# Performance work log

Measured on AMD Instinct MI355X. Metric: run time of the kernel, lower is better.

Reference implementation:

```python
import jax, jax.numpy as jnp
import numpy as np

NEG = -9.0e9  # the -9000000000.0 sentinel used by the torch code


def _masked_bidir_scores(first, second, fmask, smask):
    """Vectorized form of the BxB python double loop in score_grounding.
    first: (B,N,D), second: (B,L,D), fmask: (B,N), smask: (B,L).
    Returns sent_scores (B,B) and mention_scores (B,N,L) (= diagonal att)."""
    mask = fmask[:, None, :, None] * smask[None, :, None, :]          # (B,B,N,L)
    avg = jnp.where(mask != 0, mask, NEG)
    am_first = jax.nn.softmax(avg, axis=2)                            # softmax over N (dim=0 per pair)
    am_second = jax.nn.softmax(avg, axis=3)                           # softmax over L (dim=1 per pair)
    dot = jnp.einsum('ind,jld->ijnl', first, second)                  # (B,B,N,L)
    attm = dot * mask
    att = jnp.where(attm * mask != 0, attm, NEG)
    aw_first = jax.nn.softmax(att, axis=3) * mask                     # softmax(att, dim=-1)*mask
    aw_second = jnp.transpose(
        jax.nn.softmax(jnp.swapaxes(att, 2, 3), axis=3) * jnp.swapaxes(mask, 2, 3), (0, 1, 3, 2)
    )                                                                 # softmax(att.T,-1)*mask.T, transposed back
    sent = (jnp.sum(aw_first * att * am_first, axis=(2, 3))
            + jnp.sum(aw_second * att * am_second, axis=(2, 3)))      # (B,B)
    B = first.shape[0]
    mention = att[jnp.arange(B), jnp.arange(B)]                       # diagonal pairs (B,N,L)
    return sent, mention


def _pairwise_mlp(first, second, W1, b1, W2, b2, W3, b3):
    # SimplePairWiseClassifier: MLP over cat(first, second, first*second); dropout=0 (eval-deterministic)
    x = jnp.concatenate([first, second, first * second], axis=-1)     # (..., 3D)
    h = jax.nn.relu(x @ W1 + b1)
    h = jax.nn.relu(h @ W2 + b2)
    return (h @ W3 + b3)[..., 0]


def setup_inputs() -> dict:
    key = jax.random.key(0)
    ks = jax.random.split(key, 12)
    B, Nt, Ns, L, D, H = 32, 64, 48, 36, 1024, 1024

    def mask(k, n):
        m = (jax.random.uniform(k, (B, n)) < 0.85).astype(jnp.float32)
        return m.at[:, :2].set(1.0)  # guarantee no all-zero rows

    return {
        'text_embeddings': jax.random.normal(ks[0], (B, Nt, D), jnp.float32),
        'span_embeddings': jax.random.normal(ks[1], (B, Ns, D), jnp.float32),
        'image_embeddings': jax.random.normal(ks[2], (B, L, D), jnp.float32),
        'text_mask': mask(ks[3], Nt),
        'span_mask': mask(ks[4], Ns),
        'image_mask': mask(ks[5], L),
        'W1': jax.random.normal(ks[6], (3 * D, H), jnp.float32) * 0.02,
        'b1': jnp.zeros((H,), jnp.float32),
        'W2': jax.random.normal(ks[7], (H, H), jnp.float32) * 0.02,
        'b2': jnp.zeros((H,), jnp.float32),
        'W3': jax.random.normal(ks[8], (H, 1), jnp.float32) * 0.02,
        'b3': jnp.zeros((1,), jnp.float32),
    }


def reference(text_embeddings, span_embeddings, image_embeddings,
              text_mask, span_mask, image_mask, W1, b1, W2, b2, W3, b3):
    B, Ns, D = span_embeddings.shape
    # calculate_loss
    S, _ = _masked_bidir_scores(text_embeddings, image_embeddings, text_mask, image_mask)
    # span_emb.view(B, N, -1, D).mean(dim=2) is identity for (B,Ns,D)
    _, grounding_scores = _masked_bidir_scores(span_embeddings, image_embeddings, span_mask, image_mask)
    # score_text over all span pairs (itertools.combinations order == triu_indices k=1)
    fi, si = np.triu_indices(Ns, k=1)
    text_scores = _pairwise_mlp(span_embeddings[:, fi], span_embeddings[:, si],
                                W1, b1, W2, b2, W3, b3)               # (B, Ns*(Ns-1)/2)
    # contrastive retrieval loss over the BxB sentence-image score matrix
    loss = -(jnp.trace(jax.nn.log_softmax(S, axis=1))
             + jnp.trace(jax.nn.log_softmax(S.T, axis=1))) / B
    return loss, grounding_scores, text_scores
```

## Files before the change

kernel.cpp:

```cpp
#include <hip/hip_runtime.h>
#include <math.h>
#include <stdint.h>

#define B_    32
#define NT    64
#define NS    48
#define LI    36
#define D_    1024
#define H_    1024
#define NPAIR 1128
#define ROWS  (B_*NPAIR)
#define NEGV  -9.0e9f

typedef _Float16 half8 __attribute__((ext_vector_type(8)));
typedef float floatx4 __attribute__((ext_vector_type(4)));
typedef __attribute__((address_space(3))) uint32_t lds_u32;
typedef __attribute__((address_space(1))) const uint32_t glb_u32;

#define GLOAD16(src, dst) __builtin_amdgcn_global_load_lds((glb_u32*)(src), (lds_u32*)(dst), 16, 0, 0)

#define MMQ(QR, QC)                                                            \
  {                                                                            \
    _Pragma("unroll") for (int i = 0; i < 4; ++i) {                            \
      _Pragma("unroll") for (int j = 0; j < 2; ++j) {                          \
        acc[QR * 4 + i][QC * 2 + j] = __builtin_amdgcn_mfma_f32_16x16x32_f16(  \
            aF[i][0], bF[j][0], acc[QR * 4 + i][QC * 2 + j], 0, 0, 0);         \
        acc[QR * 4 + i][QC * 2 + j] = __builtin_amdgcn_mfma_f32_16x16x32_f16(  \
            aF[i][1], bF[j][1], acc[QR * 4 + i][QC * 2 + j], 0, 0, 0);         \
      }                                                                        \
    }                                                                          \
  }

__global__ __launch_bounds__(512, 2) void gemm1_8ph(
    const _Float16* __restrict__ spanH, const _Float16* __restrict__ W1cT,
    const float* __restrict__ AB1, const float* __restrict__ b1,
    _Float16* __restrict__ h1out,
    const int* __restrict__ idxF, const int* __restrict__ idxS) {
  __shared__ __align__(16) _Float16 sP[32768];
  __shared__ int sIF[256], sIS[256];

  const int orig = blockIdx.x;
  const int xcd = orig & 7, pos = orig >> 3;
  const int wg = (xcd < 4 ? xcd * 71 : 284 + (xcd - 4) * 70) + pos;
  const int rowBase = (wg >> 2) * 256;
  const int colBase = (wg & 3) * 256;

  const int t = threadIdx.x;
  const int wave = t >> 6, lane = t & 63;
  const int wq_r = wave >> 2, wq_c = wave & 3;
  const int l15 = lane & 15, l16 = lane >> 4;

  if (t < 256) { sIF[t] = idxF[rowBase + t]; sIS[t] = idxS[rowBase + t]; }
  __syncthreads();

  const int srow = t >> 3;
  const int slot = t & 7;
  const int wsw = ((slot ^ (srow & 7)) << 3);

  const int oF0a = sIF[srow] << 10,        oF0b = sIF[64 + srow] << 10;
  const int oS0a = sIS[srow] << 10,        oS0b = sIS[64 + srow] << 10;
  const int oF1a = sIF[128 + srow] << 10,  oF1b = sIF[192 + srow] << 10;
  const int oS1a = sIS[128 + srow] << 10,  oS1b = sIS[192 + srow] << 10;
  const int lcol = slot << 3;

  const _Float16* gB0a = W1cT + (size_t)(colBase + srow) * D_ + wsw;
  const _Float16* gB0b = W1cT + (size_t)(colBase + 64 + srow) * D_ + wsw;
  const _Float16* gB1a = W1cT + (size_t)(colBase + 128 + srow) * D_ + wsw;
  const _Float16* gB1b = W1cT + (size_t)(colBase + 192 + srow) * D_ + wsw;

  half8 rF0a, rF0b, rS0a, rS0b, rF1a, rF1b, rS1a, rS1b;

  #define ISSUE_FS0(kt) {                                            \
    const int kc = (((kt) & 15) << 6) + lcol;                        \
    rF0a = *(const half8*)(spanH + oF0a + kc);                       \
    rF0b = *(const half8*)(spanH + oF0b + kc);                       \
    rS0a = *(const half8*)(spanH + oS0a + kc);                       \
    rS0b = *(const half8*)(spanH + oS0b + kc); }
  #define ISSUE_FS1(kt) {                                            \
    const int kc = (((kt) & 15) << 6) + lcol;                        \
    rF1a = *(const half8*)(spanH + oF1a + kc);                       \
    rF1b = *(const half8*)(spanH + oF1b + kc);                       \
    rS1a = *(const half8*)(spanH + oS1a + kc);                       \
    rS1b = *(const half8*)(spanH + oS1b + kc); }
  #define WRITE_A0() {                                               \
    *(half8*)(sP + srow * 64 + wsw)        = rF0a * rS0a;            \
    *(half8*)(sP + 4096 + srow * 64 + wsw) = rF0b * rS0b; }
  #define WRITE_A1() {                                               \
    *(half8*)(sP + 8192 + srow * 64 + wsw)  = rF1a * rS1a;           \
    *(half8*)(sP + 12288 + srow * 64 + wsw) = rF1b * rS1b; }
  #define STG_B0(kt) {                                               \
    const int kc = (((kt) & 15) << 6);                               \
    GLOAD16(gB0a + kc, sP + 16384 + t * 8);                          \
    GLOAD16(gB0b + kc, sP + 20480 + t * 8); }
  #define STG_B1(kt) {                                               \
    const int kc = (((kt) & 15) << 6);                               \
    GLOAD16(gB1a + kc, sP + 24576 + t * 8);                          \
    GLOAD16(gB1b + kc, sP + 28672 + t * 8); }

  const int rsw = l15 & 7;
  const int aRd = (wq_r * 64 + l15) * 64;
  const int bRd = (wq_c * 32 + l15) * 64;
  const int rd0 = ((l16) ^ rsw) << 3;
  const int rd1 = ((4 + l16) ^ rsw) << 3;
  half8 aF[4][2], bF[2][2];
  floatx4 acc[8][4] = {};
  #define LDA(h) {                                                   \
    const _Float16* p = sP + (h) * 8192 + aRd;                       \
    _Pragma("unroll") for (int i = 0; i < 4; ++i) {                  \
      aF[i][0] = *(const half8*)(p + i * 1024 + rd0);                \
      aF[i][1] = *(const half8*)(p + i * 1024 + rd1); } }
  #define LDB(h) {                                                   \
    const _Float16* p = sP + 16384 + (h) * 8192 + bRd;               \
    _Pragma("unroll") for (int j = 0; j < 2; ++j) {                  \
      bF[j][0] = *(const half8*)(p + j * 1024 + rd0);                \
      bF[j][1] = *(const half8*)(p + j * 1024 + rd1); } }

  ISSUE_FS0(0); ISSUE_FS1(0); STG_B0(0);
  asm volatile("s_waitcnt vmcnt(6)" ::: "memory");
  WRITE_A0();
  asm volatile("s_waitcnt lgkmcnt(0)" ::: "memory");
  __builtin_amdgcn_sched_barrier(0);
  __builtin_amdgcn_s_barrier();

#pragma unroll 1
  for (int kt = 0; kt < 16; ++kt) {
    STG_B1(kt);
    ISSUE_FS0(kt + 1);
    asm volatile("s_waitcnt vmcnt(6)" ::: "memory");
    WRITE_A1();
    LDA(0); LDB(0);
    asm volatile("s_waitcnt lgkmcnt(0)" ::: "memory");
    __builtin_amdgcn_sched_barrier(0);
    __builtin_amdgcn_s_barrier();
    __builtin_amdgcn_s_setprio(1);
    MMQ(0, 0);
    __builtin_amdgcn_s_setprio(0);
    __builtin_amdgcn_s_barrier();
    ISSUE_FS1(kt + 1);
    LDA(1);
    __builtin_amdgcn_sched_barrier(0);
    __builtin_amdgcn_s_barrier();
    __builtin_amdgcn_s_setprio(1);
    MMQ(1, 0);
    __builtin_amdgcn_s_setprio(0);
    __builtin_amdgcn_s_barrier();
    STG_B0(kt + 1);
    asm volatile("s_waitcnt vmcnt(10)" ::: "memory");
    LDA(0); LDB(1);
    __builtin_amdgcn_sched_barrier(0);
    __builtin_amdgcn_s_barrier();
    __builtin_amdgcn_s_setprio(1);
    MMQ(0, 1);
    __builtin_amdgcn_s_setprio(0);
    __builtin_amdgcn_s_barrier();
    asm volatile("s_waitcnt vmcnt(6)" ::: "memory");
    WRITE_A0();
    LDA(1);
    asm volatile("s_waitcnt lgkmcnt(0)" ::: "memory");
    __builtin_amdgcn_sched_barrier(0);
    __builtin_amdgcn_s_barrier();
    __builtin_amdgcn_s_setprio(1);
    MMQ(1, 1);
    __builtin_amdgcn_s_setprio(0);
    __builtin_amdgcn_s_barrier();
  }

  float bv[2][2];
#pragma unroll
  for (int qc = 0; qc < 2; ++qc)
#pragma unroll
    for (int j = 0; j < 2; ++j)
      bv[qc][j] = b1[colBase + qc * 128 + wq_c * 32 + j * 16 + l15];
#pragma unroll
  for (int qr = 0; qr < 2; ++qr)
#pragma unroll
    for (int i = 0; i < 4; ++i)
#pragma unroll
      for (int q = 0; q < 4; ++q) {
        int rL = qr * 128 + wq_r * 64 + i * 16 + l16 * 4 + q;
        const float* ap = AB1 + (size_t)sIF[rL] * 2048;
        const float* bp = AB1 + (size_t)sIS[rL] * 2048 + 1024;
        size_t ro = (size_t)(rowBase + rL) * 1024;
#pragma unroll
        for (int qc = 0; qc < 2; ++qc)
#pragma unroll
          for (int j = 0; j < 2; ++j) {
            int c = colBase + qc * 128 + wq_c * 32 + j * 16 + l15;
            float v = acc[qr * 4 + i][qc * 2 + j][q] + ap[c] + bp[c] + bv[qc][j];
            h1out[ro + c] = (_Float16)fmaxf(v, 0.f);
          }
      }
}

__global__ __launch_bounds__(512, 2) void gemm2_8ph(
    const _Float16* __restrict__ Am, const _Float16* __restrict__ Bt,
    float* __restrict__ scores, const float* __restrict__ bias,
    const float* __restrict__ W3) {
  __shared__ __align__(16) _Float16 sP[65536];
  __shared__ float sRed[256][4];

  const int orig = blockIdx.x;
  const int xcd = orig & 7, pos = orig >> 3;
  const int wg = (xcd < 4 ? xcd * 71 : 284 + (xcd - 4) * 70) + pos;
  const int rowBase = (wg >> 2) * 256;
  const int colBase = (wg & 3) * 256;

  const int t = threadIdx.x;
  const int wave = t >> 6, lane = t & 63;
  const int wq_r = wave >> 2, wq_c = wave & 3;
  const int l15 = lane & 15, l16 = lane >> 4;
  const int sxor = l15 & 7;

  const int srow0 = t >> 3, srow1 = (512 + t) >> 3;
  const int lcol0 = ((t & 7) ^ (srow0 & 7)) << 3;
  const int lcol1 = (((512 + t) & 7) ^ (srow1 & 7)) << 3;
  const _Float16* aS0 = Am + (size_t)(rowBase + srow0) * D_ + lcol0;
  const _Float16* aS1 = Am + (size_t)(rowBase + srow1) * D_ + lcol1;
  const _Float16* bS0 = Bt + (size_t)(colBase + srow0) * D_ + lcol0;
  const _Float16* bS1 = Bt + (size_t)(colBase + srow1) * D_ + lcol1;

  auto stgA = [&](int kt, int h) {
    const int db = kt & 1;
    const size_t so = (size_t)(kt & 15) * 64 + (size_t)h * 128 * D_;
    _Float16* d = sP + ((db << 1) + h) * 8192;
    GLOAD16(aS0 + so, d + t * 8);
    GLOAD16(aS1 + so, d + 4096 + t * 8);
  };
  auto stgB = [&](int kt, int h) {
    const int db = kt & 1;
    const size_t so = (size_t)(kt & 15) * 64 + (size_t)h * 128 * D_;
    _Float16* d = sP + 32768 + ((db << 1) + h) * 8192;
    GLOAD16(bS0 + so, d + t * 8);
    GLOAD16(bS1 + so, d + 4096 + t * 8);
  };

  const int aRdRow = (wq_r * 64 + l15) * 64;
  const int bRdRow = (wq_c * 32 + l15) * 64;
  const int rdSlot0 = ((l16) ^ sxor) << 3;
  const int rdSlot1 = ((4 + l16) ^ sxor) << 3;

  half8 aF[4][2], bF[2][2];
  floatx4 acc[8][4] = {};

  auto ldA = [&](int db, int qr) {
    const _Float16* p = sP + ((db << 1) + qr) * 8192 + aRdRow;
#pragma unroll
    for (int i = 0; i < 4; ++i) {
      aF[i][0] = *(const half8*)(p + i * 1024 + rdSlot0);
      aF[i][1] = *(const half8*)(p + i * 1024 + rdSlot1);
    }
  };
  auto ldB = [&](int db, int qc) {
    const _Float16* p = sP + 32768 + ((db << 1) + qc) * 8192 + bRdRow;
#pragma unroll
    for (int j = 0; j < 2; ++j) {
      bF[j][0] = *(const half8*)(p + j * 1024 + rdSlot0);
      bF[j][1] = *(const half8*)(p + j * 1024 + rdSlot1);
    }
  };

  stgB(0, 0); stgA(0, 1); stgA(0, 0); stgB(0, 1); stgB(1, 0); stgA(1, 1);
  asm volatile("s_waitcnt vmcnt(4)" ::: "memory");
  __builtin_amdgcn_s_barrier();

#pragma unroll 1
  for (int kt = 0; kt < 16; ++kt) {
    const int db = kt & 1;
    const int kn1 = kt + 1, kn2 = kt + 2;
    ldA(db, 0); ldB(db, 0);
    stgA(kn1, 0);
    __builtin_amdgcn_sched_barrier(0);
    __builtin_amdgcn_s_barrier();
    __builtin_amdgcn_s_setprio(1);
    MMQ(0, 0);
    __builtin_amdgcn_s_setprio(0);
    __builtin_amdgcn_s_barrier();
    ldA(db, 1);
    stgB(kn1, 1);
    __builtin_amdgcn_sched_barrier(0);
    __builtin_amdgcn_s_barrier();
    __builtin_amdgcn_s_setprio(1);
    MMQ(1, 0);
    __builtin_amdgcn_s_setprio(0);
    __builtin_amdgcn_s_barrier();
    ldB(db, 1);
    stgB(kn2, 0);
    __builtin_amdgcn_sched_barrier(0);
    __builtin_amdgcn_s_barrier();
    __builtin_amdgcn_s_setprio(1);
    MMQ(1, 1);
    __builtin_amdgcn_s_setprio(0);
    __builtin_amdgcn_s_barrier();
    ldA(db, 0);
    stgA(kn2, 1);
    __builtin_amdgcn_sched_barrier(0);
    asm volatile("s_waitcnt vmcnt(4)" ::: "memory");
    __builtin_amdgcn_s_barrier();
    __builtin_amdgcn_s_setprio(1);
    MMQ(0, 1);
    __builtin_amdgcn_s_setprio(0);
    __builtin_amdgcn_s_barrier();
  }

  float bv[2][2], wv[2][2];
#pragma unroll
  for (int qc = 0; qc < 2; ++qc)
#pragma unroll
    for (int j = 0; j < 2; ++j) {
      int c = colBase + qc * 128 + wq_c * 32 + j * 16 + l15;
      bv[qc][j] = bias[c];
      wv[qc][j] = W3[c];
    }
#pragma unroll
  for (int qr = 0; qr < 2; ++qr)
#pragma unroll
    for (int i = 0; i < 4; ++i)
#pragma unroll
      for (int q = 0; q < 4; ++q) {
        float s = 0.f;
#pragma unroll
        for (int qc = 0; qc < 2; ++qc)
#pragma unroll
          for (int j = 0; j < 2; ++j)
            s += fmaxf(acc[qr * 4 + i][qc * 2 + j][q] + bv[qc][j], 0.f) * wv[qc][j];
        s += __shfl_xor(s, 1); s += __shfl_xor(s, 2);
        s += __shfl_xor(s, 4); s += __shfl_xor(s, 8);
        if (l15 == 0)
          sRed[qr * 128 + wq_r * 64 + i * 16 + l16 * 4 + q][wq_c] = s;
      }
  __syncthreads();
  if (t < 256)
    atomicAdd(&scores[rowBase + t],
              sRed[t][0] + sRed[t][1] + sRed[t][2] + sRed[t][3]);
}

__device__ __forceinline__ void gemm_body(
    const _Float16* __restrict__ A, const _Float16* __restrict__ Bt,
    float* __restrict__ Cf, int N, int K, int rowBase, int colBase) {
  __shared__ __align__(16) _Float16 sA[8192];
  __shared__ __align__(16) _Float16 sB[8192];
  const int tid = threadIdx.x;
  const int lane = tid & 63;
  const int wave = tid >> 6;
  const int wr = wave >> 1, wc = wave & 1;
  const int l15 = lane & 15, l16 = lane >> 4;
  const int rsw = (l15 >> 1) & 3;
  const int sRow = tid >> 2;
  const int swz8 = (((tid & 3) ^ ((tid >> 3) & 3)) << 3);
  const _Float16* gA = A + (size_t)(rowBase + sRow) * K + swz8;
  const _Float16* gB = Bt + (size_t)(colBase + sRow) * K + swz8;
  _Float16* lA = sA + tid * 8;
  _Float16* lB = sB + tid * 8;

  floatx4 acc[4][4] = {};
  for (int k0 = 0; k0 < K; k0 += 64) {
    GLOAD16(gA + k0,               lA);
    GLOAD16(gA + 64 * K + k0,      lA + 2048);
    GLOAD16(gA + k0 + 32,          lA + 4096);
    GLOAD16(gA + 64 * K + k0 + 32, lA + 6144);
    GLOAD16(gB + k0,               lB);
    GLOAD16(gB + 64 * K + k0,      lB + 2048);
    GLOAD16(gB + k0 + 32,          lB + 4096);
    GLOAD16(gB + 64 * K + k0 + 32, lB + 6144);
    __syncthreads();
#pragma unroll
    for (int h = 0; h < 2; ++h) {
      const int hb = h * 4096;
      half8 aF[4], bF[4];
#pragma unroll
      for (int i = 0; i < 4; ++i)
        aF[i] = *(const half8*)&sA[hb + (wr * 64 + i * 16 + l15) * 32 + ((l16 ^ rsw) << 3)];
#pragma unroll
      for (int j = 0; j < 4; ++j)
        bF[j] = *(const half8*)&sB[hb + (wc * 64 + j * 16 + l15) * 32 + ((l16 ^ rsw) << 3)];
#pragma unroll
      for (int i = 0; i < 4; ++i)
#pragma unroll
        for (int j = 0; j < 4; ++j)
          acc[i][j] = __builtin_amdgcn_mfma_f32_16x16x32_f16(aF[i], bF[j], acc[i][j], 0, 0, 0);
    }
    __syncthreads();
  }
#pragma unroll
  for (int i = 0; i < 4; ++i)
#pragma unroll
    for (int q = 0; q < 4; ++q) {
      int r = rowBase + wr * 64 + i * 16 + l16 * 4 + q;
#pragma unroll
      for (int j = 0; j < 4; ++j) {
        int c = colBase + wc * 64 + j * 16 + l15;
        Cf[(size_t)r * N + c] = acc[i][j][q];
      }
    }
}

__global__ __launch_bounds__(256) void gemm_trio(
    const _Float16* __restrict__ textH, const _Float16* __restrict__ imgH,
    const _Float16* __restrict__ spanH, const _Float16* __restrict__ W1abT,
    float* __restrict__ dotTI, float* __restrict__ dotSI, float* __restrict__ AB1) {
  int bid = blockIdx.x;
  if (bid < 144)      gemm_body(textH, imgH, dotTI, 1152, D_, (bid / 9) * 128, (bid % 9) * 128);
  else if (bid < 252) { int b = bid - 144; gemm_body(spanH, imgH, dotSI, 1152, D_, (b / 9) * 128, (b % 9) * 128); }
  else                { int b = bid - 252; gemm_body(spanH, W1abT, AB1, 2048, D_, (b / 16) * 128, (b % 16) * 128); }
}

__global__ __launch_bounds__(256) void cvt_all(
    const float* __restrict__ text, const float* __restrict__ span,
    const float* __restrict__ img, _Float16* __restrict__ textH,
    _Float16* __restrict__ spanH, _Float16* __restrict__ imgH) {
  long long i = (long long)blockIdx.x * 256 + threadIdx.x;
  const float* src; _Float16* dst; long long off;
  if (i < 262144)      { src = text; dst = textH; off = i; }
  else if (i < 458752) { src = span; dst = spanH; off = i - 262144; }
  else if (i < 606208) { src = img;  dst = imgH;  off = i - 458752; }
  else return;
  const float4* p = (const float4*)src + off * 2;
  float4 a = p[0], b = p[1];
  half8 h;
  h[0] = (_Float16)a.x; h[1] = (_Float16)a.y; h[2] = (_Float16)a.z; h[3] = (_Float16)a.w;
  h[4] = (_Float16)b.x; h[5] = (_Float16)b.y; h[6] = (_Float16)b.z; h[7] = (_Float16)b.w;
  *(half8*)(dst + off * 8) = h;
}

__global__ __launch_bounds__(256) void transpose_all(
    const float* __restrict__ W1, const float* __restrict__ W2,
    _Float16* __restrict__ W1abT, _Float16* __restrict__ W1cT,
    _Float16* __restrict__ W2T) {
  __shared__ float tbuf[32][33];
  const float* in; _Float16* out;
  switch (blockIdx.z) {
    case 0: in = W1;                 out = W1abT;                 break;
    case 1: in = W1 + 1024 * 1024;   out = W1abT + 1024 * 1024;   break;
    case 2: in = W1 + 2048 * 1024;   out = W1cT;                  break;
    default: in = W2;                out = W2T;                   break;
  }
  const int tx = threadIdx.x & 31, ty = threadIdx.x >> 5;
  const int k0 = blockIdx.y * 32, n0 = blockIdx.x * 32;
#pragma unroll
  for (int q = 0; q < 4; ++q)
    tbuf[ty + q * 8][tx] = in[(size_t)(k0 + ty + q * 8) * 1024 + n0 + tx];
  __syncthreads();
#pragma unroll
  for (int q = 0; q < 4; ++q)
    out[(size_t)(n0 + ty + q * 8) * 1024 + k0 + tx] = (_Float16)tbuf[tx][ty + q * 8];
}

__global__ __launch_bounds__(256) void idx_init(int* __restrict__ idxF, int* __restrict__ idxS) {
  int r = blockIdx.x * 256 + threadIdx.x;
  if (r >= ROWS) return;
  int bb = r / NPAIR, p = r - bb * NPAIR;
  int cum = 0, f = 0;
  while (true) { int cnt = NS - 1 - f; if (p < cum + cnt) break; cum += cnt; ++f; }
  idxF[r] = bb * NS + f;
  idxS[r] = bb * NS + f + 1 + (p - cum);
}

__global__ void init_scores(float* __restrict__ scores, const float* __restrict__ b3) {
  int idx = blockIdx.x * 256 + threadIdx.x;
  if (idx < ROWS) scores[idx] = b3[0];
}

__global__ __launch_bounds__(256) void extract_grounding(
    const float* __restrict__ dotSI, const float* __restrict__ smask,
    const float* __restrict__ imask, float* __restrict__ outg) {
  int idx = blockIdx.x * 256 + threadIdx.x;
  if (idx >= B_ * NS * LI) return;
  int b = idx / (NS * LI);
  int rem = idx - b * (NS * LI);
  int n = rem / LI, l = rem - n * LI;
  float v = dotSI[(size_t)(b * NS + n) * (B_ * LI) + b * LI + l];
  outg[idx] = (smask[b * NS + n] * imask[b * LI + l] != 0.f) ? v : NEGV;
}

__global__ __launch_bounds__(64) void sent_kernel(
    const float* __restrict__ dotTI, const float* __restrict__ tmask,
    const float* __restrict__ imask, float* __restrict__ S) {
  const int i = blockIdx.y, j = blockIdx.x, t = threadIdx.x;
  __shared__ float red1[64], red2[64];
  const int stride = B_ * LI;
  float e1 = 0.f;
  {
    float tm = tmask[i * NT + t];
    if (tm != 0.f) {
      const float* row = dotTI + (size_t)(i * NT + t) * stride + j * LI;
      float m = -INFINITY;
      for (int l = 0; l < LI; ++l) if (imask[j * LI + l] != 0.f) m = fmaxf(m, row[l]);
      float z = 0.f, w = 0.f;
      for (int l = 0; l < LI; ++l) if (imask[j * LI + l] != 0.f) {
        float d = row[l], p = expf(d - m);
        z += p; w += p * d;
      }
      e1 = w / z;
    }
  }
  red1[t] = e1;
  float e2 = 0.f;
  if (t < LI) {
    float im = imask[j * LI + t];
    if (im != 0.f) {
      const float* col = dotTI + (size_t)(i * NT) * stride + j * LI + t;
      float m = -INFINITY;
      for (int n = 0; n < NT; ++n) if (tmask[i * NT + n] != 0.f) m = fmaxf(m, col[(size_t)n * stride]);
      float z = 0.f, w = 0.f;
      for (int n = 0; n < NT; ++n) if (tmask[i * NT + n] != 0.f) {
        float d = col[(size_t)n * stride], p = expf(d - m);
        z += p; w += p * d;
      }
      e2 = w / z;
    }
  }
  red2[t] = e2;
  __syncthreads();
  if (t == 0) {
    float s1 = 0.f, s2 = 0.f, cn = 0.f, cl = 0.f;
    for (int n = 0; n < NT; ++n) { s1 += red1[n]; cn += tmask[i * NT + n]; }
    for (int l = 0; l < LI; ++l) { s2 += red2[l]; cl += imask[j * LI + l]; }
    S[i * B_ + j] = s1 / cn + s2 / cl;
  }
}

__global__ __launch_bounds__(64) void loss_kernel(
    const float* __restrict__ S, float* __restrict__ out) {
  __shared__ float sS[B_][B_ + 1];
  __shared__ float acc[B_];
  const int t = threadIdx.x;
  for (int e = t; e < B_ * B_; e += 64) sS[e / B_][e % B_] = S[e];
  __syncthreads();
  if (t < B_) {
    float m = -INFINITY;
    for (int j = 0; j < B_; ++j) m = fmaxf(m, sS[t][j]);
    float z = 0.f;
    for (int j = 0; j < B_; ++j) z += expf(sS[t][j] - m);
    float lr = m + logf(z);
    float m2 = -INFINITY;
    for (int i = 0; i < B_; ++i) m2 = fmaxf(m2, sS[i][t]);
    float z2 = 0.f;
    for (int i = 0; i < B_; ++i) z2 += expf(sS[i][t] - m2);
    float lc = m2 + logf(z2);
    acc[t] = 2.f * sS[t][t] - lr - lc;
  }
  __syncthreads();
  if (t == 0) {
    float s = 0.f;
    for (int i = 0; i < B_; ++i) s += acc[i];
    out[0] = -s / (float)B_;
  }
}

extern "C" void kernel_launch(void* const* d_in, const int* in_sizes, int n_in,
                              void* d_out, int out_size, void* d_ws, size_t ws_size,
                              hipStream_t stream) {
  const float* text  = (const float*)d_in[0];
  const float* span  = (const float*)d_in[1];
  const float* img   = (const float*)d_in[2];
  const float* tmask = (const float*)d_in[3];
  const float* smask = (const float*)d_in[4];
  const float* imask = (const float*)d_in[5];
  const float* W1    = (const float*)d_in[6];
  const float* b1    = (const float*)d_in[7];
  const float* W2    = (const float*)d_in[8];
  const float* b2    = (const float*)d_in[9];
  const float* W3    = (const float*)d_in[10];
  const float* b3    = (const float*)d_in[11];

  float* out     = (float*)d_out;
  float* outLoss = out;
  float* outG    = out + 1;
  float* outT    = out + 1 + (size_t)B_ * NS * LI;

  char* w = (char*)d_ws;
  float*    dotTI = (float*)w;            w += (size_t)(B_*NT) * (B_*LI) * 4;
  float*    dotSI = (float*)w;            w += (size_t)(B_*NS) * (B_*LI) * 4;
  float*    S     = (float*)w;            w += 1024 * 4;
  float*    AB1   = (float*)w;            w += (size_t)1536 * 2048 * 4;
  _Float16* h1    = (_Float16*)w;         w += (size_t)ROWS * 1024 * 2;
  _Float16* textH = (_Float16*)w;         w += (size_t)2048 * 1024 * 2;
  _Float16* spanH = (_Float16*)w;         w += (size_t)1536 * 1024 * 2;
  _Float16* imgH  = (_Float16*)w;         w += (size_t)1152 * 1024 * 2;
  _Float16* W1abT = (_Float16*)w;         w += (size_t)2048 * 1024 * 2;
  _Float16* W1cT  = (_Float16*)w;         w += (size_t)1024 * 1024 * 2;
  _Float16* W2T   = (_Float16*)w;         w += (size_t)1024 * 1024 * 2;
  int*      idxF  = (int*)w;              w += ROWS * 4;
  int*      idxS  = (int*)w;              w += ROWS * 4;
  (void)ws_size; (void)in_sizes; (void)n_in; (void)out_size;

  cvt_all<<<(606208 + 255) / 256, 256, 0, stream>>>(text, span, img, textH, spanH, imgH);
  transpose_all<<<dim3(32, 32, 4), 256, 0, stream>>>(W1, W2, W1abT, W1cT, W2T);
  idx_init<<<(ROWS + 255) / 256, 256, 0, stream>>>(idxF, idxS);

  gemm_trio<<<444, 256, 0, stream>>>(textH, imgH, spanH, W1abT, dotTI, dotSI, AB1);
  sent_kernel<<<dim3(B_, B_), 64, 0, stream>>>(dotTI, tmask, imask, S);
  loss_kernel<<<1, 64, 0, stream>>>(S, outLoss);
  extract_grounding<<<(B_*NS*LI + 255) / 256, 256, 0, stream>>>(dotSI, smask, imask, outG);

  gemm1_8ph<<<564, 512, 0, stream>>>(spanH, W1cT, AB1, b1, h1, idxF, idxS);
  init_scores<<<(ROWS + 255) / 256, 256, 0, stream>>>(outT, b3);
  gemm2_8ph<<<564, 512, 0, stream>>>(h1, W2T, outT, b2, W3);
}
```

Before: 350.0 us.

## Double-buffer LDS tiles in gemm1 to overlap next k-tile loads with MFMA

Doubles the shared-memory staging buffer in the gather-product GEMM so the A (product of gathered span rows) and B (W1 slice) tiles for k-tile kt+1 are written while k-tile kt is consumed. The quadrant MFMA order and wait counts are reorganised around that double buffer, which is meant to hide global load latency behind the matrix work. The cost is 128KB of LDS per block, which likely breaks the launch_bounds(512,2) occupancy of two blocks per CU. The loop also reads and stages tiles past kt=15 (masked with &15), which adds a little redundant traffic.

```diff
diff --git a/kernel.cpp b/kernel.cpp
--- a/kernel.cpp
+++ b/kernel.cpp
@@ -36,7 +36,7 @@
     const float* __restrict__ AB1, const float* __restrict__ b1,
     _Float16* __restrict__ h1out,
     const int* __restrict__ idxF, const int* __restrict__ idxS) {
-  __shared__ __align__(16) _Float16 sP[32768];
+  __shared__ __align__(16) _Float16 sP[65536];
   __shared__ int sIF[256], sIS[256];
 
   const int orig = blockIdx.x;
@@ -49,6 +49,7 @@
   const int wave = t >> 6, lane = t & 63;
   const int wq_r = wave >> 2, wq_c = wave & 3;
   const int l15 = lane & 15, l16 = lane >> 4;
+  const int sxor = l15 & 7;
 
   if (t < 256) { sIF[t] = idxF[rowBase + t]; sIS[t] = idxS[rowBase + t]; }
   __syncthreads();
@@ -56,17 +57,11 @@
   const int srow = t >> 3;
   const int slot = t & 7;
   const int wsw = ((slot ^ (srow & 7)) << 3);
-
-  const int oF0a = sIF[srow] << 10,        oF0b = sIF[64 + srow] << 10;
-  const int oS0a = sIS[srow] << 10,        oS0b = sIS[64 + srow] << 10;
-  const int oF1a = sIF[128 + srow] << 10,  oF1b = sIF[192 + srow] << 10;
-  const int oS1a = sIS[128 + srow] << 10,  oS1b = sIS[192 + srow] << 10;
   const int lcol = slot << 3;
-
-  const _Float16* gB0a = W1cT + (size_t)(colBase + srow) * D_ + wsw;
-  const _Float16* gB0b = W1cT + (size_t)(colBase + 64 + srow) * D_ + wsw;
-  const _Float16* gB1a = W1cT + (size_t)(colBase + 128 + srow) * D_ + wsw;
-  const _Float16* gB1b = W1cT + (size_t)(colBase + 192 + srow) * D_ + wsw;
+  const int oF0a = sIF[srow] << 10,       oF0b = sIF[64 + srow] << 10;
+  const int oS0a = sIS[srow] << 10,       oS0b = sIS[64 + srow] << 10;
+  const int oF1a = sIF[128 + srow] << 10, oF1b = sIF[192 + srow] << 10;
+  const int oS1a = sIS[128 + srow] << 10, oS1b = sIS[192 + srow] << 10;
 
   half8 rF0a, rF0b, rS0a, rS0b, rF1a, rF1b, rS1a, rS1b;
 
@@ -82,85 +77,90 @@
     rF1b = *(const half8*)(spanH + oF1b + kc);                       \
     rS1a = *(const half8*)(spanH + oS1a + kc);                       \
     rS1b = *(const half8*)(spanH + oS1b + kc); }
-  #define WRITE_A0() {                                               \
-    *(half8*)(sP + srow * 64 + wsw)        = rF0a * rS0a;            \
-    *(half8*)(sP + 4096 + srow * 64 + wsw) = rF0b * rS0b; }
-  #define WRITE_A1() {                                               \
-    *(half8*)(sP + 8192 + srow * 64 + wsw)  = rF1a * rS1a;           \
-    *(half8*)(sP + 12288 + srow * 64 + wsw) = rF1b * rS1b; }
-  #define STG_B0(kt) {                                               \
-    const int kc = (((kt) & 15) << 6);                               \
-    GLOAD16(gB0a + kc, sP + 16384 + t * 8);                          \
-    GLOAD16(gB0b + kc, sP + 20480 + t * 8); }
-  #define STG_B1(kt) {                                               \
-    const int kc = (((kt) & 15) << 6);                               \
-    GLOAD16(gB1a + kc, sP + 24576 + t * 8);                          \
-    GLOAD16(gB1b + kc, sP + 28672 + t * 8); }
-
-  const int rsw = l15 & 7;
-  const int aRd = (wq_r * 64 + l15) * 64;
-  const int bRd = (wq_c * 32 + l15) * 64;
-  const int rd0 = ((l16) ^ rsw) << 3;
-  const int rd1 = ((4 + l16) ^ rsw) << 3;
+  #define WRITE_A0(kt) {                                             \
+    _Float16* d = sP + ((((kt) & 1) << 1) + 0) * 8192;               \
+    *(half8*)(d + srow * 64 + wsw)        = rF0a * rS0a;             \
+    *(half8*)(d + 4096 + srow * 64 + wsw) = rF0b * rS0b; }
+  #define WRITE_A1(kt) {                                             \
+    _Float16* d = sP + ((((kt) & 1) << 1) + 1) * 8192;               \
+    *(half8*)(d + srow * 64 + wsw)        = rF1a * rS1a;             \
+    *(half8*)(d + 4096 + srow * 64 + wsw) = rF1b * rS1b; }
+
+  const int srow0 = t >> 3, srow1 = 64 + (t >> 3);
+  const int lcol0 = ((t & 7) ^ (srow0 & 7)) << 3;
+  const int lcol1 = ((t & 7) ^ (srow1 & 7)) << 3;
+  const _Float16* bS0 = W1cT + (size_t)(colBase + srow0) * D_ + lcol0;
+  const _Float16* bS1 = W1cT + (size_t)(colBase + srow1) * D_ + lcol1;
+  #define STG_B(kt, h) {                                             \
+    const size_t so = (size_t)((kt) & 15) * 64 + (size_t)(h) * 128 * D_; \
+    _Float16* d = sP + 32768 + ((((kt) & 1) << 1) + (h)) * 8192;     \
+    GLOAD16(bS0 + so, d + t * 8);                                    \
+    GLOAD16(bS1 + so, d + 4096 + t * 8); }
+
+  const int aRdRow = (wq_r * 64 + l15) * 64;
+  const int bRdRow = (wq_c * 32 + l15) * 64;
+  const int rd0 = ((l16) ^ sxor) << 3;
+  const int rd1 = ((4 + l16) ^ sxor) << 3;
   half8 aF[4][2], bF[2][2];
   floatx4 acc[8][4] = {};
-  #define LDA(h) {                                                   \
-    const _Float16* p = sP + (h) * 8192 + aRd;                       \
+  #define LDA(db, h) {                                               \
+    const _Float16* p = sP + (((db) << 1) + (h)) * 8192 + aRdRow;    \
     _Pragma("unroll") for (int i = 0; i < 4; ++i) {                  \
       aF[i][0] = *(const half8*)(p + i * 1024 + rd0);                \
       aF[i][1] = *(const half8*)(p + i * 1024 + rd1); } }
-  #define LDB(h) {                                                   \
-    const _Float16* p = sP + 16384 + (h) * 8192 + bRd;               \
+  #define LDB(db, h) {                                               \
+    const _Float16* p = sP + 32768 + (((db) << 1) + (h)) * 8192 + bRdRow; \
     _Pragma("unroll") for (int j = 0; j < 2; ++j) {                  \
       bF[j][0] = *(const half8*)(p + j * 1024 + rd0);                \
       bF[j][1] = *(const half8*)(p + j * 1024 + rd1); } }
 
-  ISSUE_FS0(0); ISSUE_FS1(0); STG_B0(0);
-  asm volatile("s_waitcnt vmcnt(6)" ::: "memory");
-  WRITE_A0();
+  ISSUE_FS0(0); ISSUE_FS1(0);
+  STG_B(0, 0); STG_B(0, 1);
+  WRITE_A0(0);
+  WRITE_A1(0);
+  ISSUE_FS0(1); ISSUE_FS1(1);
+  asm volatile("s_waitcnt vmcnt(8)" ::: "memory");
   asm volatile("s_waitcnt lgkmcnt(0)" ::: "memory");
   __builtin_amdgcn_sched_barrier(0);
   __builtin_amdgcn_s_barrier();
 
 #pragma unroll 1
   for (int kt = 0; kt < 16; ++kt) {
-    STG_B1(kt);
-    ISSUE_FS0(kt + 1);
-    asm volatile("s_waitcnt vmcnt(6)" ::: "memory");
-    WRITE_A1();
-    LDA(0); LDB(0);
+    const int db = kt & 1;
+    LDA(db, 0); LDB(db, 0);
+    STG_B(kt + 1, 0);
+    __builtin_amdgcn_sched_barrier(0);
+    __builtin_amdgcn_s_barrier();
+    __builtin_amdgcn_s_setprio(1);
+    MMQ(0, 0);
+    __builtin_amdgcn_s_setprio(0);
+    __builtin_amdgcn_s_barrier();
+    LDA(db, 1);
+    STG_B(kt + 1, 1);
+    __builtin_amdgcn_sched_barrier(0);
+    __builtin_amdgcn_s_barrier();
+    __builtin_amdgcn_s_setprio(1);
+    MMQ(1, 0);
+    __builtin_amdgcn_s_setprio(0);
+    __builtin_amdgcn_s_barrier();
+    WRITE_A0(kt + 1);
+    ISSUE_FS0(kt + 2);
+    LDB(db, 1);
+    __builtin_amdgcn_sched_barrier(0);
+    __builtin_amdgcn_s_barrier();
+    __builtin_amdgcn_s_setprio(1);
+    MMQ(1, 1);
+    __builtin_amdgcn_s_setprio(0);
+    __builtin_amdgcn_s_barrier();
+    WRITE_A1(kt + 1);
+    ISSUE_FS1(kt + 2);
+    LDA(db, 0);
+    asm volatile("s_waitcnt vmcnt(8)" ::: "memory");
     asm volatile("s_waitcnt lgkmcnt(0)" ::: "memory");
     __builtin_amdgcn_sched_barrier(0);
     __builtin_amdgcn_s_barrier();
     __builtin_amdgcn_s_setprio(1);
-    MMQ(0, 0);
-    __builtin_amdgcn_s_setprio(0);
-    __builtin_amdgcn_s_barrier();
-    ISSUE_FS1(kt + 1);
-    LDA(1);
-    __builtin_amdgcn_sched_barrier(0);
-    __builtin_amdgcn_s_barrier();
-    __builtin_amdgcn_s_setprio(1);
-    MMQ(1, 0);
-    __builtin_amdgcn_s_setprio(0);
-    __builtin_amdgcn_s_barrier();
-    STG_B0(kt + 1);
-    asm volatile("s_waitcnt vmcnt(10)" ::: "memory");
-    LDA(0); LDB(1);
-    __builtin_amdgcn_sched_barrier(0);
-    __builtin_amdgcn_s_barrier();
-    __builtin_amdgcn_s_setprio(1);
     MMQ(0, 1);
-    __builtin_amdgcn_s_setprio(0);
-    __builtin_amdgcn_s_barrier();
-    asm volatile("s_waitcnt vmcnt(6)" ::: "memory");
-    WRITE_A0();
-    LDA(1);
-    asm volatile("s_waitcnt lgkmcnt(0)" ::: "memory");
-    __builtin_amdgcn_sched_barrier(0);
-    __builtin_amdgcn_s_barrier();
-    __builtin_amdgcn_s_setprio(1);
-    MMQ(1, 1);
     __builtin_amdgcn_s_setprio(0);
     __builtin_amdgcn_s_barrier();
   }
```

Result: no change. 344.8 us (-1.5%).
